# Optimization experiments

Hardware: AMD Instinct MI355X
Metric: run time of the kernel (lower is better)

## Reference

```python
import jax, jax.numpy as jnp
import numpy as np

B = 4096
ED = 128          # EMBEDDING_DIM
HD = 64           # HIDDEN_DIM
LH = 128          # LSTM_HIDDEN_DIM
IN_DIM = ED * (12 + 48 + 1)  # 7808
N_ABILITY, N_MOVE = 300, 900


def setup_inputs() -> dict:
    key = jax.random.key(0)
    ks = jax.random.split(key, 16)
    s = lambda k, shape, scale=0.05: (jax.random.normal(k, shape, dtype=jnp.float32) * scale)
    return {
        "ability_ids": jax.random.randint(ks[0], (B, 12), 0, N_ABILITY),
        "move_ids": jax.random.randint(ks[1], (B, 48), 0, N_MOVE),
        "numerical": s(ks[2], (B, 84), 1.0),
        "mask": (jax.random.uniform(ks[3], (B, 9)) > 0.3).astype(jnp.float32),
        "h0": jnp.zeros((B, LH), jnp.float32),
        "c0": jnp.zeros((B, LH), jnp.float32),
        "ability_emb": s(ks[4], (N_ABILITY, ED), 1.0),
        "move_emb": s(ks[5], (N_MOVE, ED), 1.0),
        "num_W": s(ks[6], (ED, 84)),
        "num_b": s(ks[7], (ED,)),
        "Wih": s(ks[8], (4 * LH, IN_DIM), 0.01),
        "Whh": s(ks[9], (4 * LH, LH)),
        "bih": s(ks[10], (4 * LH,)),
        "bhh": s(ks[11], (4 * LH,)),
        "W1": s(ks[12], (HD, LH)),
        "b1": s(ks[13], (HD,)),
        "W2": s(ks[14], (ED, HD)),
        "b2": s(ks[15], (ED,)),
        "Wa": s(jax.random.fold_in(key, 100), (9, ED)),
        "ba": s(jax.random.fold_in(key, 101), (9,)),
    }


def reference(ability_ids, move_ids, numerical, mask, h0, c0,
              ability_emb, move_emb, num_W, num_b,
              Wih, Whh, bih, bhh, W1, b1, W2, b2, Wa, ba):
    # Gather + concat: [B, 12*ED] + [B, 48*ED] + [B, ED] -> [B, 7808]
    ab = ability_emb[ability_ids].reshape(ability_ids.shape[0], 12 * ED)
    mv = move_emb[move_ids].reshape(move_ids.shape[0], 48 * ED)
    num = numerical @ num_W.T + num_b
    x = jnp.concatenate([ab, mv, num], axis=-1)

    # Single-timestep LSTM (torch gate order: i, f, g, o)
    gates = x @ Wih.T + bih + h0 @ Whh.T + bhh
    i, f, g, o = jnp.split(gates, 4, axis=-1)
    i, f, o = jax.nn.sigmoid(i), jax.nn.sigmoid(f), jax.nn.sigmoid(o)
    g = jnp.tanh(g)
    c1 = f * c0 + i * g
    h1 = o * jnp.tanh(c1)

    # MLP head + action logits
    feat = jax.nn.relu(h1 @ W1.T + b1) @ W2.T + b2
    probs = jax.nn.softmax(feat @ Wa.T + ba, axis=-1)

    # Masked renormalization; fall back to unmasked probs when mask kills everything
    masked = probs * mask
    ssum = masked.sum(-1, keepdims=True)
    out = jnp.where(ssum > 0, masked / jnp.where(ssum > 0, ssum, 1.0), probs)
    return out, h1, c1
```

## Files before the change

### kernel.cpp

```cpp
#include <hip/hip_runtime.h>
#include <hip/hip_bf16.h>
#include <stdint.h>
#include <stddef.h>

typedef __bf16 bf16;
typedef __bf16 bf16x8 __attribute__((ext_vector_type(8)));
typedef float f32x4 __attribute__((ext_vector_type(4)));

#define BATCH 4096
#define KIH 7808
#define KTOT 7936
#define NG 512
#define LH 128
#define HD 64
#define ED 128
#define SPLITK 4

#define OFF_WCAT 0u
#define OFF_GPART 8126464u
#define OFF_XT   41680896u
#define OFF_AB   43778048u
#define OFF_MV   43854848u
#define OFF_ADDR 44085248u
#define OFF_H1B  46182400u

#define O_H1 (BATCH * 9)
#define O_C1 (BATCH * 9 + BATCH * LH)

typedef const __attribute__((address_space(1))) uint32_t* gas_ptr;
typedef __attribute__((address_space(3))) uint32_t* las_ptr;

__device__ __forceinline__ void async16(const void* g, void* l) {
    __builtin_amdgcn_global_load_lds((gas_ptr)g, (las_ptr)l, 16, 0, 0);
}

__global__ void convert_w(const float* __restrict__ Wih,
                          const float* __restrict__ Whh,
                          bf16* __restrict__ Wcat) {
    const int n = blockIdx.x;
    const int t = threadIdx.x;
    const float* src_ih = Wih + (size_t)n * KIH;
    const float* src_hh = Whh + (size_t)n * LH;
    bf16* dst = Wcat + (size_t)n * KTOT;
    for (int k4 = t; k4 < KTOT / 4; k4 += 256) {
        const int k = k4 * 4;
        const float4 v = (k < KIH) ? *(const float4*)(src_ih + k)
                                   : *(const float4*)(src_hh + (k - KIH));
        bf16 o0 = (bf16)v.x, o1 = (bf16)v.y, o2 = (bf16)v.z, o3 = (bf16)v.w;
        dst[k] = o0; dst[k + 1] = o1; dst[k + 2] = o2; dst[k + 3] = o3;
    }
}

__global__ void convert_emb(const float* __restrict__ ab_emb,
                            const float* __restrict__ mv_emb,
                            bf16* __restrict__ ab8,
                            bf16* __restrict__ mv8) {
    const int i = blockIdx.x * 256 + threadIdx.x;
    if (i < 300 * 128) ab8[i] = (bf16)ab_emb[i];
    else mv8[i - 300 * 128] = (bf16)mv_emb[i - 300 * 128];
}

__global__ void build_pre(const int* __restrict__ ab_ids,
                          const int* __restrict__ mv_ids,
                          const float* __restrict__ numerical,
                          const float* __restrict__ h0,
                          const float* __restrict__ numW,
                          const float* __restrict__ numb,
                          bf16* __restrict__ xtail,
                          uint32_t* __restrict__ addrs) {
    const int b = blockIdx.x;
    const int t = threadIdx.x;

    __shared__ int ids[60];
    __shared__ float numr[84];
    if (t < 60) ids[t] = (t < 12) ? ab_ids[b * 12 + t] : mv_ids[b * 48 + (t - 12)];
    if (t >= 128 && t < 128 + 84) numr[t - 128] = numerical[(size_t)b * 84 + (t - 128)];
    __syncthreads();

    if (t < 128) {
        float acc = numb[t];
#pragma unroll 4
        for (int k = 0; k < 84; ++k)
            acc += numr[k] * numW[t * 84 + k];
        xtail[(size_t)b * 256 + t] = (bf16)acc;
    } else {
        const int tt = t - 128;
        xtail[(size_t)b * 256 + 128 + tt] = (bf16)h0[(size_t)b * LH + tt];
    }

    if (t < 64) {
        uint32_t off;
        if (t < 12) off = OFF_AB + (uint32_t)ids[t] * 256u;
        else if (t < 60) off = OFF_MV + (uint32_t)ids[t] * 256u;
        else if (t == 60) off = OFF_XT + (uint32_t)b * 512u;
        else if (t == 61) off = OFF_XT + (uint32_t)b * 512u + 256u;
        else off = OFF_XT;
        addrs[(size_t)b * 64 + t] = off;
    }
}

__global__ __launch_bounds__(256, 2) void gemm_gates(
    const uint8_t* __restrict__ wsbase,
    const bf16* __restrict__ Wcat,
    const uint32_t* __restrict__ addrs,
    float* __restrict__ gpart) {
    __shared__ bf16 As[2][128 * 64];
    __shared__ bf16 Bs[2][128 * 64];
    __shared__ uint32_t adr[17][128];

    const int tid = threadIdx.x;
    const int w = tid >> 6;
    const int lane = tid & 63;
    const int bm = blockIdx.x;
    const int bn = blockIdx.y;
    const int bz = blockIdx.z;
    const int kt_beg = bz * 31;
    const int kt_end = kt_beg + 31;

    const int s0 = kt_beg >> 1;
    const int ns = ((kt_end - 1) >> 1) - s0 + 1;
    for (int i = tid; i < ns * 128; i += 256) {
        adr[i >> 7][i & 127] =
            addrs[(size_t)(bm * 128 + (i & 127)) * 64 + s0 + (i >> 7)];
    }

    const int r_l = lane >> 3;
    const int sc16 = ((lane & 7) ^ r_l) * 16;

    f32x4 acc[4][4];
#pragma unroll
    for (int i = 0; i < 4; ++i)
#pragma unroll
        for (int j = 0; j < 4; ++j)
#pragma unroll
            for (int r = 0; r < 4; ++r) acc[i][j][r] = 0.f;

    const int m0 = (w & 1) * 64;
    const int n0 = (w >> 1) * 64;

    __syncthreads();

    auto stage = [&](int kt, int pb) {
        const int k0 = kt * 64;
        const int sl = (kt >> 1) - s0;
        const int hb = (kt & 1) * 128;
#pragma unroll
        for (int j = 0; j < 4; ++j) {
            const int row = (w * 4 + j) * 8 + r_l;
            const uint8_t* gsrc = wsbase + adr[sl][row] + hb + sc16;
            async16(gsrc, (void*)&As[pb][((w * 4 + j) * 64 + lane) * 8]);
        }
#pragma unroll
        for (int j = 0; j < 4; ++j) {
            const int row = (w * 4 + j) * 8 + r_l;
            const bf16* gsrc = Wcat + (size_t)(bn * 128 + row) * KTOT + k0 + (sc16 >> 1);
            async16(gsrc, (void*)&Bs[pb][((w * 4 + j) * 64 + lane) * 8]);
        }
    };

    stage(kt_beg, 0);

    for (int kt = kt_beg; kt < kt_end; ++kt) {
        const int pb = (kt - kt_beg) & 1;
        __syncthreads();
        if (kt + 1 < kt_end) stage(kt + 1, pb ^ 1);

        const bf16* Ab = &As[pb][0];
        const bf16* Bb = &Bs[pb][0];
#pragma unroll
        for (int ks = 0; ks < 2; ++ks) {
            bf16x8 af[4], bfr[4];
            const int kk8 = ks * 4 + (lane >> 4);
#pragma unroll
            for (int t = 0; t < 4; ++t) {
                const int m = m0 + t * 16 + (lane & 15);
                af[t] = *(const bf16x8*)&Ab[m * 64 + ((kk8 ^ (m & 7)) * 8)];
                const int n = n0 + t * 16 + (lane & 15);
                bfr[t] = *(const bf16x8*)&Bb[n * 64 + ((kk8 ^ (n & 7)) * 8)];
            }
#pragma unroll
            for (int ti = 0; ti < 4; ++ti)
#pragma unroll
                for (int tj = 0; tj < 4; ++tj)
                    acc[ti][tj] = __builtin_amdgcn_mfma_f32_16x16x32_bf16(
                        af[ti], bfr[tj], acc[ti][tj], 0, 0, 0);
        }
    }

    float* gdst = gpart + (size_t)bz * BATCH * NG;
    const int mlo = (lane >> 4) * 4;
    const int nlo = lane & 15;
#pragma unroll
    for (int ti = 0; ti < 4; ++ti)
#pragma unroll
        for (int tj = 0; tj < 4; ++tj) {
            const int mg = bm * 128 + m0 + ti * 16 + mlo;
            const int ng = bn * 128 + n0 + tj * 16 + nlo;
            float* dst = gdst + (size_t)mg * NG + ng;
#pragma unroll
            for (int r = 0; r < 4; ++r)
                dst[(size_t)r * NG] = acc[ti][tj][r];
        }
}

__global__ void reduce_lstm(const float* __restrict__ gpart,
                            const float* __restrict__ bih,
                            const float* __restrict__ bhh,
                            const float* __restrict__ c0,
                            float* __restrict__ out,
                            bf16* __restrict__ h1b) {
    const int t = threadIdx.x;
    const int b = blockIdx.x * 2 + (t >> 7);
    const int u = t & 127;

    float gv[4];
#pragma unroll
    for (int q = 0; q < 4; ++q)
        gv[q] = bih[q * 128 + u] + bhh[q * 128 + u];
#pragma unroll
    for (int z = 0; z < SPLITK; ++z) {
        const float* gz = gpart + ((size_t)z * BATCH + b) * NG + u;
#pragma unroll
        for (int q = 0; q < 4; ++q) gv[q] += gz[q * 128];
    }

    const float iv = 1.f / (1.f + __expf(-gv[0]));
    const float fv = 1.f / (1.f + __expf(-gv[1]));
    const float gg = tanhf(gv[2]);
    const float ov = 1.f / (1.f + __expf(-gv[3]));
    const float c1 = fv * c0[(size_t)b * LH + u] + iv * gg;
    const float h1 = ov * tanhf(c1);

    out[O_H1 + (size_t)b * LH + u] = h1;
    out[O_C1 + (size_t)b * LH + u] = c1;
    h1b[(size_t)b * LH + u] = (bf16)h1;
}

__global__ __launch_bounds__(128, 2) void mlp_head(
    const bf16* __restrict__ h1b, const float* __restrict__ mask,
    const float* __restrict__ W1, const float* __restrict__ b1,
    const float* __restrict__ W2, const float* __restrict__ b2,
    const float* __restrict__ Wa, const float* __restrict__ ba,
    float* __restrict__ out) {
    __shared__ bf16 W1f[8192];
    __shared__ bf16 W2f[8192];
    __shared__ bf16 Waf[2048];
    __shared__ bf16 uS[2][16 * 64];
    __shared__ bf16 fS[2][16 * 128];
    __shared__ float b1s[64];
    __shared__ float b2s[128];
    __shared__ float bas[16];

    const int tid = threadIdx.x;
    for (int e = tid; e < 8192; e += 128) {
        const int j = e & 7, ln = (e >> 3) & 63, fid = e >> 9;
        const int kt = fid & 3, nt = fid >> 2;
        const int n = nt * 16 + (ln & 15);
        const int k = kt * 32 + (ln >> 4) * 8 + j;
        W1f[e] = (bf16)W1[n * 128 + k];
    }
    for (int e = tid; e < 8192; e += 128) {
        const int j = e & 7, ln = (e >> 3) & 63, fid = e >> 9;
        const int kt = fid & 1, nt = fid >> 1;
        const int n = nt * 16 + (ln & 15);
        const int k = kt * 32 + (ln >> 4) * 8 + j;
        W2f[e] = (bf16)W2[n * 64 + k];
    }
    for (int e = tid; e < 2048; e += 128) {
        const int j = e & 7, ln = (e >> 3) & 63, kt = e >> 9;
        const int n = ln & 15;
        const int k = kt * 32 + (ln >> 4) * 8 + j;
        Waf[e] = (n < 9) ? (bf16)Wa[n * 128 + k] : (bf16)0.f;
    }
    if (tid < 64) b1s[tid] = b1[tid];
    if (tid < 16) bas[tid] = (tid < 9) ? ba[tid] : 0.f;
    {
        const int i = tid;
        if (i < 128) b2s[i] = b2[i];
    }
    __syncthreads();

    const int wv = tid >> 6, lane = tid & 63;
    const int mt = blockIdx.x * 2 + wv;
    const int mrow0 = mt * 16;
    const int nl = lane & 15, kg = lane >> 4;

    bf16x8 ah[4];
#pragma unroll
    for (int kt = 0; kt < 4; ++kt)
        ah[kt] = *(const bf16x8*)&h1b[(size_t)(mrow0 + nl) * 128 + kt * 32 + kg * 8];

#pragma unroll
    for (int nt = 0; nt < 4; ++nt) {
        f32x4 a = {0.f, 0.f, 0.f, 0.f};
#pragma unroll
        for (int kt = 0; kt < 4; ++kt)
            a = __builtin_amdgcn_mfma_f32_16x16x32_bf16(
                ah[kt], *(const bf16x8*)&W1f[((nt * 4 + kt) * 64 + lane) * 8], a, 0, 0, 0);
        const int n = nt * 16 + nl;
#pragma unroll
        for (int r = 0; r < 4; ++r)
            uS[wv][(kg * 4 + r) * 64 + n] = (bf16)fmaxf(a[r] + b1s[n], 0.f);
    }

    bf16x8 au[2];
#pragma unroll
    for (int kt = 0; kt < 2; ++kt)
        au[kt] = *(const bf16x8*)&uS[wv][nl * 64 + kt * 32 + kg * 8];

#pragma unroll
    for (int nt = 0; nt < 8; ++nt) {
        f32x4 a = {0.f, 0.f, 0.f, 0.f};
#pragma unroll
        for (int kt = 0; kt < 2; ++kt)
            a = __builtin_amdgcn_mfma_f32_16x16x32_bf16(
                au[kt], *(const bf16x8*)&W2f[((nt * 2 + kt) * 64 + lane) * 8], a, 0, 0, 0);
        const int n = nt * 16 + nl;
#pragma unroll
        for (int r = 0; r < 4; ++r)
            fS[wv][(kg * 4 + r) * 128 + n] = (bf16)(a[r] + b2s[n]);
    }

    bf16x8 afr[4];
#pragma unroll
    for (int kt = 0; kt < 4; ++kt)
        afr[kt] = *(const bf16x8*)&fS[wv][nl * 128 + kt * 32 + kg * 8];

    f32x4 lg4 = {0.f, 0.f, 0.f, 0.f};
#pragma unroll
    for (int kt = 0; kt < 4; ++kt)
        lg4 = __builtin_amdgcn_mfma_f32_16x16x32_bf16(
            afr[kt], *(const bf16x8*)&Waf[(kt * 64 + lane) * 8], lg4, 0, 0, 0);

#pragma unroll
    for (int r = 0; r < 4; ++r) {
        const int b = mrow0 + kg * 4 + r;
        float lg = (nl < 9) ? lg4[r] + bas[nl] : -1e30f;
        float mx = lg;
#pragma unroll
        for (int off = 1; off < 16; off <<= 1)
            mx = fmaxf(mx, __shfl_xor(mx, off, 64));
        const float e = (nl < 9) ? __expf(lg - mx) : 0.f;
        const float mv = (nl < 9) ? mask[(size_t)b * 9 + nl] : 0.f;
        float tot = e, ms = e * mv;
#pragma unroll
        for (int off = 1; off < 16; off <<= 1) {
            tot += __shfl_xor(tot, off, 64);
            ms += __shfl_xor(ms, off, 64);
        }
        if (nl < 9)
            out[(size_t)b * 9 + nl] = (ms > 0.f) ? e * mv / ms : e / tot;
    }
}

extern "C" void kernel_launch(void* const* d_in, const int* in_sizes, int n_in,
                              void* d_out, int out_size, void* d_ws, size_t ws_size,
                              hipStream_t stream) {
    const int* ab_ids = (const int*)d_in[0];
    const int* mv_ids = (const int*)d_in[1];
    const float* numerical = (const float*)d_in[2];
    const float* mask = (const float*)d_in[3];
    const float* h0 = (const float*)d_in[4];
    const float* c0 = (const float*)d_in[5];
    const float* ab_emb = (const float*)d_in[6];
    const float* mv_emb = (const float*)d_in[7];
    const float* numW = (const float*)d_in[8];
    const float* numb = (const float*)d_in[9];
    const float* Wih = (const float*)d_in[10];
    const float* Whh = (const float*)d_in[11];
    const float* bih = (const float*)d_in[12];
    const float* bhh = (const float*)d_in[13];
    const float* W1 = (const float*)d_in[14];
    const float* b1 = (const float*)d_in[15];
    const float* W2 = (const float*)d_in[16];
    const float* b2 = (const float*)d_in[17];
    const float* Wa = (const float*)d_in[18];
    const float* ba = (const float*)d_in[19];
    float* out = (float*)d_out;

    uint8_t* ws = (uint8_t*)d_ws;
    bf16* Wcat = (bf16*)(ws + OFF_WCAT);
    float* gpart = (float*)(ws + OFF_GPART);
    bf16* xtail = (bf16*)(ws + OFF_XT);
    bf16* ab8 = (bf16*)(ws + OFF_AB);
    bf16* mv8 = (bf16*)(ws + OFF_MV);
    uint32_t* addrs = (uint32_t*)(ws + OFF_ADDR);
    bf16* h1b = (bf16*)(ws + OFF_H1B);

    convert_w<<<512, 256, 0, stream>>>(Wih, Whh, Wcat);
    convert_emb<<<600, 256, 0, stream>>>(ab_emb, mv_emb, ab8, mv8);
    build_pre<<<BATCH, 256, 0, stream>>>(ab_ids, mv_ids, numerical, h0,
                                         numW, numb, xtail, addrs);
    gemm_gates<<<dim3(32, 4, SPLITK), 256, 0, stream>>>(ws, Wcat, addrs, gpart);
    reduce_lstm<<<BATCH / 2, 256, 0, stream>>>(gpart, bih, bhh, c0, out, h1b);
    mlp_head<<<128, 128, 0, stream>>>(h1b, mask, W1, b1, W2, b2, Wa, ba, out);
}
```

Before: 190.7 us.

## Merge prep kernels, enlarge GEMM M-tile, fuse LSTM reduce into MLP head

Merges the three preprocessing kernels (weight convert, embedding convert, build_pre) into one launch that dispatches on block index. The gates GEMM moves to 512-thread blocks with a 256-row M tile, so each B tile is reused across twice as many rows. The split-K reduction and LSTM cell are fused into the MLP head kernel, which keeps h1 in shared memory instead of writing it to workspace. This removes launch overhead and a global round trip. The cost is more shared memory and registers per GEMM block, and a tail kernel of only 256 blocks that redoes the weight staging in each block.

```diff
diff --git a/kernel.cpp b/kernel.cpp
--- a/kernel.cpp
+++ b/kernel.cpp
@@ -22,7 +22,6 @@
 #define OFF_AB   43778048u
 #define OFF_MV   43854848u
 #define OFF_ADDR 44085248u
-#define OFF_H1B  46182400u
 
 #define O_H1 (BATCH * 9)
 #define O_C1 (BATCH * 9 + BATCH * LH)
@@ -34,79 +33,81 @@
     __builtin_amdgcn_global_load_lds((gas_ptr)g, (las_ptr)l, 16, 0, 0);
 }
 
-__global__ void convert_w(const float* __restrict__ Wih,
-                          const float* __restrict__ Whh,
-                          bf16* __restrict__ Wcat) {
-    const int n = blockIdx.x;
+__global__ void prep(const int* __restrict__ ab_ids,
+                     const int* __restrict__ mv_ids,
+                     const float* __restrict__ numerical,
+                     const float* __restrict__ h0,
+                     const float* __restrict__ numW,
+                     const float* __restrict__ numb,
+                     const float* __restrict__ Wih,
+                     const float* __restrict__ Whh,
+                     const float* __restrict__ ab_emb,
+                     const float* __restrict__ mv_emb,
+                     uint8_t* __restrict__ ws) {
+    const int bid = blockIdx.x;
     const int t = threadIdx.x;
-    const float* src_ih = Wih + (size_t)n * KIH;
-    const float* src_hh = Whh + (size_t)n * LH;
-    bf16* dst = Wcat + (size_t)n * KTOT;
-    for (int k4 = t; k4 < KTOT / 4; k4 += 256) {
-        const int k = k4 * 4;
-        const float4 v = (k < KIH) ? *(const float4*)(src_ih + k)
-                                   : *(const float4*)(src_hh + (k - KIH));
-        bf16 o0 = (bf16)v.x, o1 = (bf16)v.y, o2 = (bf16)v.z, o3 = (bf16)v.w;
-        dst[k] = o0; dst[k + 1] = o1; dst[k + 2] = o2; dst[k + 3] = o3;
-    }
-}
-
-__global__ void convert_emb(const float* __restrict__ ab_emb,
-                            const float* __restrict__ mv_emb,
-                            bf16* __restrict__ ab8,
-                            bf16* __restrict__ mv8) {
-    const int i = blockIdx.x * 256 + threadIdx.x;
-    if (i < 300 * 128) ab8[i] = (bf16)ab_emb[i];
-    else mv8[i - 300 * 128] = (bf16)mv_emb[i - 300 * 128];
-}
-
-__global__ void build_pre(const int* __restrict__ ab_ids,
-                          const int* __restrict__ mv_ids,
-                          const float* __restrict__ numerical,
-                          const float* __restrict__ h0,
-                          const float* __restrict__ numW,
-                          const float* __restrict__ numb,
-                          bf16* __restrict__ xtail,
-                          uint32_t* __restrict__ addrs) {
-    const int b = blockIdx.x;
-    const int t = threadIdx.x;
-
-    __shared__ int ids[60];
-    __shared__ float numr[84];
-    if (t < 60) ids[t] = (t < 12) ? ab_ids[b * 12 + t] : mv_ids[b * 48 + (t - 12)];
-    if (t >= 128 && t < 128 + 84) numr[t - 128] = numerical[(size_t)b * 84 + (t - 128)];
-    __syncthreads();
-
-    if (t < 128) {
-        float acc = numb[t];
+
+    if (bid < BATCH) {
+        bf16* xtail = (bf16*)(ws + OFF_XT);
+        uint32_t* addrs = (uint32_t*)(ws + OFF_ADDR);
+        const int b = bid;
+
+        __shared__ int ids[60];
+        __shared__ float numr[84];
+        if (t < 60) ids[t] = (t < 12) ? ab_ids[b * 12 + t] : mv_ids[b * 48 + (t - 12)];
+        if (t >= 128 && t < 128 + 84) numr[t - 128] = numerical[(size_t)b * 84 + (t - 128)];
+        __syncthreads();
+
+        if (t < 128) {
+            float acc = numb[t];
 #pragma unroll 4
-        for (int k = 0; k < 84; ++k)
-            acc += numr[k] * numW[t * 84 + k];
-        xtail[(size_t)b * 256 + t] = (bf16)acc;
+            for (int k = 0; k < 84; ++k)
+                acc += numr[k] * numW[t * 84 + k];
+            xtail[(size_t)b * 256 + t] = (bf16)acc;
+        } else {
+            const int tt = t - 128;
+            xtail[(size_t)b * 256 + 128 + tt] = (bf16)h0[(size_t)b * LH + tt];
+        }
+
+        if (t < 64) {
+            uint32_t off;
+            if (t < 12) off = OFF_AB + (uint32_t)ids[t] * 256u;
+            else if (t < 60) off = OFF_MV + (uint32_t)ids[t] * 256u;
+            else if (t == 60) off = OFF_XT + (uint32_t)b * 512u;
+            else if (t == 61) off = OFF_XT + (uint32_t)b * 512u + 256u;
+            else off = OFF_XT;
+            addrs[(size_t)b * 64 + t] = off;
+        }
+    } else if (bid < BATCH + 512) {
+        bf16* Wcat = (bf16*)(ws + OFF_WCAT);
+        const int n = bid - BATCH;
+        const float* src_ih = Wih + (size_t)n * KIH;
+        const float* src_hh = Whh + (size_t)n * LH;
+        bf16* dst = Wcat + (size_t)n * KTOT;
+        for (int k4 = t; k4 < KTOT / 4; k4 += 256) {
+            const int k = k4 * 4;
+            const float4 v = (k < KIH) ? *(const float4*)(src_ih + k)
+                                       : *(const float4*)(src_hh + (k - KIH));
+            bf16 o0 = (bf16)v.x, o1 = (bf16)v.y, o2 = (bf16)v.z, o3 = (bf16)v.w;
+            dst[k] = o0; dst[k + 1] = o1; dst[k + 2] = o2; dst[k + 3] = o3;
+        }
     } else {
-        const int tt = t - 128;
-        xtail[(size_t)b * 256 + 128 + tt] = (bf16)h0[(size_t)b * LH + tt];
-    }
-
-    if (t < 64) {
-        uint32_t off;
-        if (t < 12) off = OFF_AB + (uint32_t)ids[t] * 256u;
-        else if (t < 60) off = OFF_MV + (uint32_t)ids[t] * 256u;
-        else if (t == 60) off = OFF_XT + (uint32_t)b * 512u;
-        else if (t == 61) off = OFF_XT + (uint32_t)b * 512u + 256u;
-        else off = OFF_XT;
-        addrs[(size_t)b * 64 + t] = off;
-    }
-}
-
-__global__ __launch_bounds__(256, 2) void gemm_gates(
+        bf16* ab8 = (bf16*)(ws + OFF_AB);
+        bf16* mv8 = (bf16*)(ws + OFF_MV);
+        const int i = (bid - BATCH - 512) * 256 + t;
+        if (i < 300 * 128) ab8[i] = (bf16)ab_emb[i];
+        else if (i < 1200 * 128) mv8[i - 300 * 128] = (bf16)mv_emb[i - 300 * 128];
+    }
+}
+
+__global__ __launch_bounds__(512, 2) void gemm_gates(
     const uint8_t* __restrict__ wsbase,
     const bf16* __restrict__ Wcat,
     const uint32_t* __restrict__ addrs,
     float* __restrict__ gpart) {
-    __shared__ bf16 As[2][128 * 64];
+    __shared__ bf16 As[2][256 * 64];
     __shared__ bf16 Bs[2][128 * 64];
-    __shared__ uint32_t adr[17][128];
+    __shared__ uint32_t adr[16][256];
 
     const int tid = threadIdx.x;
     const int w = tid >> 6;
@@ -119,9 +120,9 @@
 
     const int s0 = kt_beg >> 1;
     const int ns = ((kt_end - 1) >> 1) - s0 + 1;
-    for (int i = tid; i < ns * 128; i += 256) {
-        adr[i >> 7][i & 127] =
-            addrs[(size_t)(bm * 128 + (i & 127)) * 64 + s0 + (i >> 7)];
+    for (int i = tid; i < ns * 256; i += 512) {
+        adr[i >> 8][i & 255] =
+            addrs[(size_t)(bm * 256 + (i & 255)) * 64 + s0 + (i >> 8)];
     }
 
     const int r_l = lane >> 3;
@@ -135,8 +136,9 @@
 #pragma unroll
             for (int r = 0; r < 4; ++r) acc[i][j][r] = 0.f;
 
-    const int m0 = (w & 1) * 64;
-    const int n0 = (w >> 1) * 64;
+    const int wm = w & 3, wn = w >> 2;
+    const int m0 = wm * 64;
+    const int n0 = wn * 64;
 
     __syncthreads();
 
@@ -146,15 +148,17 @@
         const int hb = (kt & 1) * 128;
 #pragma unroll
         for (int j = 0; j < 4; ++j) {
-            const int row = (w * 4 + j) * 8 + r_l;
+            const int g = w * 4 + j;
+            const int row = g * 8 + r_l;
             const uint8_t* gsrc = wsbase + adr[sl][row] + hb + sc16;
-            async16(gsrc, (void*)&As[pb][((w * 4 + j) * 64 + lane) * 8]);
-        }
-#pragma unroll
-        for (int j = 0; j < 4; ++j) {
-            const int row = (w * 4 + j) * 8 + r_l;
+            async16(gsrc, (void*)&As[pb][(g * 64 + lane) * 8]);
+        }
+#pragma unroll
+        for (int j = 0; j < 2; ++j) {
+            const int g = w * 2 + j;
+            const int row = g * 8 + r_l;
             const bf16* gsrc = Wcat + (size_t)(bn * 128 + row) * KTOT + k0 + (sc16 >> 1);
-            async16(gsrc, (void*)&Bs[pb][((w * 4 + j) * 64 + lane) * 8]);
+            async16(gsrc, (void*)&Bs[pb][(g * 64 + lane) * 8]);
         }
     };
 
@@ -194,7 +198,7 @@
     for (int ti = 0; ti < 4; ++ti)
 #pragma unroll
         for (int tj = 0; tj < 4; ++tj) {
-            const int mg = bm * 128 + m0 + ti * 16 + mlo;
+            const int mg = bm * 256 + m0 + ti * 16 + mlo;
             const int ng = bn * 128 + n0 + tj * 16 + nlo;
             float* dst = gdst + (size_t)mg * NG + ng;
 #pragma unroll
@@ -203,41 +207,10 @@
         }
 }
 
-__global__ void reduce_lstm(const float* __restrict__ gpart,
-                            const float* __restrict__ bih,
-                            const float* __restrict__ bhh,
-                            const float* __restrict__ c0,
-                            float* __restrict__ out,
-                            bf16* __restrict__ h1b) {
-    const int t = threadIdx.x;
-    const int b = blockIdx.x * 2 + (t >> 7);
-    const int u = t & 127;
-
-    float gv[4];
-#pragma unroll
-    for (int q = 0; q < 4; ++q)
-        gv[q] = bih[q * 128 + u] + bhh[q * 128 + u];
-#pragma unroll
-    for (int z = 0; z < SPLITK; ++z) {
-        const float* gz = gpart + ((size_t)z * BATCH + b) * NG + u;
-#pragma unroll
-        for (int q = 0; q < 4; ++q) gv[q] += gz[q * 128];
-    }
-
-    const float iv = 1.f / (1.f + __expf(-gv[0]));
-    const float fv = 1.f / (1.f + __expf(-gv[1]));
-    const float gg = tanhf(gv[2]);
-    const float ov = 1.f / (1.f + __expf(-gv[3]));
-    const float c1 = fv * c0[(size_t)b * LH + u] + iv * gg;
-    const float h1 = ov * tanhf(c1);
-
-    out[O_H1 + (size_t)b * LH + u] = h1;
-    out[O_C1 + (size_t)b * LH + u] = c1;
-    h1b[(size_t)b * LH + u] = (bf16)h1;
-}
-
-__global__ __launch_bounds__(128, 2) void mlp_head(
-    const bf16* __restrict__ h1b, const float* __restrict__ mask,
+__global__ __launch_bounds__(128, 3) void tail(
+    const float* __restrict__ gpart, const float* __restrict__ bih,
+    const float* __restrict__ bhh, const float* __restrict__ c0,
+    const float* __restrict__ mask,
     const float* __restrict__ W1, const float* __restrict__ b1,
     const float* __restrict__ W2, const float* __restrict__ b2,
     const float* __restrict__ Wa, const float* __restrict__ ba,
@@ -245,13 +218,16 @@
     __shared__ bf16 W1f[8192];
     __shared__ bf16 W2f[8192];
     __shared__ bf16 Waf[2048];
-    __shared__ bf16 uS[2][16 * 64];
-    __shared__ bf16 fS[2][16 * 128];
+    __shared__ bf16 h1s[16 * 128];
+    __shared__ bf16 uS[16 * 64];
+    __shared__ bf16 fS[16 * 128];
     __shared__ float b1s[64];
     __shared__ float b2s[128];
     __shared__ float bas[16];
 
     const int tid = threadIdx.x;
+    const int b0 = blockIdx.x * 16;
+
     for (int e = tid; e < 8192; e += 128) {
         const int j = e & 7, ln = (e >> 3) & 63, fid = e >> 9;
         const int kt = fid & 3, nt = fid >> 2;
@@ -274,24 +250,47 @@
     }
     if (tid < 64) b1s[tid] = b1[tid];
     if (tid < 16) bas[tid] = (tid < 9) ? ba[tid] : 0.f;
-    {
-        const int i = tid;
-        if (i < 128) b2s[i] = b2[i];
+    if (tid < 128) b2s[tid] = b2[tid];
+
+#pragma unroll
+    for (int i = 0; i < 16; ++i) {
+        const int p = tid + 128 * i;
+        const int uu = p & 127;
+        const int r = p >> 7;
+        const int b = b0 + r;
+        float gv[4];
+#pragma unroll
+        for (int q = 0; q < 4; ++q)
+            gv[q] = bih[q * 128 + uu] + bhh[q * 128 + uu];
+#pragma unroll
+        for (int z = 0; z < SPLITK; ++z) {
+            const float* gz = gpart + ((size_t)z * BATCH + b) * NG + uu;
+#pragma unroll
+            for (int q = 0; q < 4; ++q) gv[q] += gz[q * 128];
+        }
+        const float iv = 1.f / (1.f + __expf(-gv[0]));
+        const float fv = 1.f / (1.f + __expf(-gv[1]));
+        const float gg = tanhf(gv[2]);
+        const float ov = 1.f / (1.f + __expf(-gv[3]));
+        const float c1 = fv * c0[(size_t)b * LH + uu] + iv * gg;
+        const float h1 = ov * tanhf(c1);
+        out[O_H1 + (size_t)b * LH + uu] = h1;
+        out[O_C1 + (size_t)b * LH + uu] = c1;
+        h1s[r * 128 + uu] = (bf16)h1;
     }
     __syncthreads();
 
     const int wv = tid >> 6, lane = tid & 63;
-    const int mt = blockIdx.x * 2 + wv;
-    const int mrow0 = mt * 16;
     const int nl = lane & 15, kg = lane >> 4;
 
     bf16x8 ah[4];
 #pragma unroll
     for (int kt = 0; kt < 4; ++kt)
-        ah[kt] = *(const bf16x8*)&h1b[(size_t)(mrow0 + nl) * 128 + kt * 32 + kg * 8];
-
-#pragma unroll
-    for (int nt = 0; nt < 4; ++nt) {
+        ah[kt] = *(const bf16x8*)&h1s[nl * 128 + kt * 32 + kg * 8];
+
+#pragma unroll
+    for (int t2 = 0; t2 < 2; ++t2) {
+        const int nt = wv * 2 + t2;
         f32x4 a = {0.f, 0.f, 0.f, 0.f};
 #pragma unroll
         for (int kt = 0; kt < 4; ++kt)
@@ -300,16 +299,18 @@
         const int n = nt * 16 + nl;
 #pragma unroll
         for (int r = 0; r < 4; ++r)
-            uS[wv][(kg * 4 + r) * 64 + n] = (bf16)fmaxf(a[r] + b1s[n], 0.f);
-    }
+            uS[(kg * 4 + r) * 64 + n] = (bf16)fmaxf(a[r] + b1s[n], 0.f);
+    }
+    __syncthreads();
 
     bf16x8 au[2];
 #pragma unroll
     for (int kt = 0; kt < 2; ++kt)
-        au[kt] = *(const bf16x8*)&uS[wv][nl * 64 + kt * 32 + kg * 8];
-
-#pragma unroll
-    for (int nt = 0; nt < 8; ++nt) {
+        au[kt] = *(const bf16x8*)&uS[nl * 64 + kt * 32 + kg * 8];
+
+#pragma unroll
+    for (int t2 = 0; t2 < 4; ++t2) {
+        const int nt = wv * 4 + t2;
         f32x4 a = {0.f, 0.f, 0.f, 0.f};
 #pragma unroll
         for (int kt = 0; kt < 2; ++kt)
@@ -318,38 +319,41 @@
         const int n = nt * 16 + nl;
 #pragma unroll
         for (int r = 0; r < 4; ++r)
-            fS[wv][(kg * 4 + r) * 128 + n] = (bf16)(a[r] + b2s[n]);
-    }
-
-    bf16x8 afr[4];
-#pragma unroll
-    for (int kt = 0; kt < 4; ++kt)
-        afr[kt] = *(const bf16x8*)&fS[wv][nl * 128 + kt * 32 + kg * 8];
-
-    f32x4 lg4 = {0.f, 0.f, 0.f, 0.f};
-#pragma unroll
-    for (int kt = 0; kt < 4; ++kt)
-        lg4 = __builtin_amdgcn_mfma_f32_16x16x32_bf16(
-            afr[kt], *(const bf16x8*)&Waf[(kt * 64 + lane) * 8], lg4, 0, 0, 0);
-
-#pragma unroll
-    for (int r = 0; r < 4; ++r) {
-        const int b = mrow0 + kg * 4 + r;
-        float lg = (nl < 9) ? lg4[r] + bas[nl] : -1e30f;
-        float mx = lg;
-#pragma unroll
-        for (int off = 1; off < 16; off <<= 1)
-            mx = fmaxf(mx, __shfl_xor(mx, off, 64));
-        const float e = (nl < 9) ? __expf(lg - mx) : 0.f;
-        const float mv = (nl < 9) ? mask[(size_t)b * 9 + nl] : 0.f;
-        float tot = e, ms = e * mv;
-#pragma unroll
-        for (int off = 1; off < 16; off <<= 1) {
-            tot += __shfl_xor(tot, off, 64);
-            ms += __shfl_xor(ms, off, 64);
-        }
-        if (nl < 9)
-            out[(size_t)b * 9 + nl] = (ms > 0.f) ? e * mv / ms : e / tot;
+            fS[(kg * 4 + r) * 128 + n] = (bf16)(a[r] + b2s[n]);
+    }
+    __syncthreads();
+
+    if (wv == 0) {
+        bf16x8 afr[4];
+#pragma unroll
+        for (int kt = 0; kt < 4; ++kt)
+            afr[kt] = *(const bf16x8*)&fS[nl * 128 + kt * 32 + kg * 8];
+
+        f32x4 lg4 = {0.f, 0.f, 0.f, 0.f};
+#pragma unroll
+        for (int kt = 0; kt < 4; ++kt)
+            lg4 = __builtin_amdgcn_mfma_f32_16x16x32_bf16(
+                afr[kt], *(const bf16x8*)&Waf[(kt * 64 + lane) * 8], lg4, 0, 0, 0);
+
+#pragma unroll
+        for (int r = 0; r < 4; ++r) {
+            const int b = b0 + kg * 4 + r;
+            float lg = (nl < 9) ? lg4[r] + bas[nl] : -1e30f;
+            float mx = lg;
+#pragma unroll
+            for (int off = 1; off < 16; off <<= 1)
+                mx = fmaxf(mx, __shfl_xor(mx, off, 64));
+            const float e = (nl < 9) ? __expf(lg - mx) : 0.f;
+            const float mv = (nl < 9) ? mask[(size_t)b * 9 + nl] : 0.f;
+            float tot = e, ms = e * mv;
+#pragma unroll
+            for (int off = 1; off < 16; off <<= 1) {
+                tot += __shfl_xor(tot, off, 64);
+                ms += __shfl_xor(ms, off, 64);
+            }
+            if (nl < 9)
+                out[(size_t)b * 9 + nl] = (ms > 0.f) ? e * mv / ms : e / tot;
+        }
     }
 }
 
@@ -381,17 +385,11 @@
     uint8_t* ws = (uint8_t*)d_ws;
     bf16* Wcat = (bf16*)(ws + OFF_WCAT);
     float* gpart = (float*)(ws + OFF_GPART);
-    bf16* xtail = (bf16*)(ws + OFF_XT);
-    bf16* ab8 = (bf16*)(ws + OFF_AB);
-    bf16* mv8 = (bf16*)(ws + OFF_MV);
     uint32_t* addrs = (uint32_t*)(ws + OFF_ADDR);
-    bf16* h1b = (bf16*)(ws + OFF_H1B);
-
-    convert_w<<<512, 256, 0, stream>>>(Wih, Whh, Wcat);
-    convert_emb<<<600, 256, 0, stream>>>(ab_emb, mv_emb, ab8, mv8);
-    build_pre<<<BATCH, 256, 0, stream>>>(ab_ids, mv_ids, numerical, h0,
-                                         numW, numb, xtail, addrs);
-    gemm_gates<<<dim3(32, 4, SPLITK), 256, 0, stream>>>(ws, Wcat, addrs, gpart);
-    reduce_lstm<<<BATCH / 2, 256, 0, stream>>>(gpart, bih, bhh, c0, out, h1b);
-    mlp_head<<<128, 128, 0, stream>>>(h1b, mask, W1, b1, W2, b2, Wa, ba, out);
-}
+
+    prep<<<BATCH + 512 + 600, 256, 0, stream>>>(
+        ab_ids, mv_ids, numerical, h0, numW, numb, Wih, Whh, ab_emb, mv_emb, ws);
+    gemm_gates<<<dim3(16, 4, SPLITK), 512, 0, stream>>>(ws, Wcat, addrs, gpart);
+    tail<<<BATCH / 16, 128, 0, stream>>>(gpart, bih, bhh, c0, mask,
+                                         W1, b1, W2, b2, Wa, ba, out);
+}
```

Result: slower. 195.3 us (+2.4%).

## Fuse preprocessing kernels and pre-swizzle MLP head weights once in workspace

Applied to the files above, without the earlier changes.

Merges the weight conversion, embedding conversion and per-row pre-build kernels into a single prep launch, dispatched by block index ranges. A dedicated block in that launch also converts and swizzles the W1/W2/Wa MLP weights into the workspace, so mlp_head no longer rebuilds them in LDS in every block. mlp_head becomes 256 single-wave blocks that read fragments straight from global memory, with bias loads from global. This removes two launches and redundant per-block weight staging, at the cost of a serial single-block weight prep and uncached global fragment reads.

```diff
diff --git a/kernel.cpp b/kernel.cpp
--- a/kernel.cpp
+++ b/kernel.cpp
@@ -23,6 +23,9 @@
 #define OFF_MV   43854848u
 #define OFF_ADDR 44085248u
 #define OFF_H1B  46182400u
+#define OFF_W1F  47230976u
+#define OFF_W2F  47247360u
+#define OFF_WAF  47263744u
 
 #define O_H1 (BATCH * 9)
 #define O_C1 (BATCH * 9 + BATCH * LH)
@@ -34,68 +37,97 @@
     __builtin_amdgcn_global_load_lds((gas_ptr)g, (las_ptr)l, 16, 0, 0);
 }
 
-__global__ void convert_w(const float* __restrict__ Wih,
-                          const float* __restrict__ Whh,
-                          bf16* __restrict__ Wcat) {
-    const int n = blockIdx.x;
+__global__ void prep(const int* __restrict__ ab_ids,
+                     const int* __restrict__ mv_ids,
+                     const float* __restrict__ numerical,
+                     const float* __restrict__ h0,
+                     const float* __restrict__ numW,
+                     const float* __restrict__ numb,
+                     const float* __restrict__ Wih,
+                     const float* __restrict__ Whh,
+                     const float* __restrict__ ab_emb,
+                     const float* __restrict__ mv_emb,
+                     const float* __restrict__ W1,
+                     const float* __restrict__ W2,
+                     const float* __restrict__ Wa,
+                     uint8_t* __restrict__ ws) {
+    const int bid = blockIdx.x;
     const int t = threadIdx.x;
-    const float* src_ih = Wih + (size_t)n * KIH;
-    const float* src_hh = Whh + (size_t)n * LH;
-    bf16* dst = Wcat + (size_t)n * KTOT;
-    for (int k4 = t; k4 < KTOT / 4; k4 += 256) {
-        const int k = k4 * 4;
-        const float4 v = (k < KIH) ? *(const float4*)(src_ih + k)
-                                   : *(const float4*)(src_hh + (k - KIH));
-        bf16 o0 = (bf16)v.x, o1 = (bf16)v.y, o2 = (bf16)v.z, o3 = (bf16)v.w;
-        dst[k] = o0; dst[k + 1] = o1; dst[k + 2] = o2; dst[k + 3] = o3;
-    }
-}
-
-__global__ void convert_emb(const float* __restrict__ ab_emb,
-                            const float* __restrict__ mv_emb,
-                            bf16* __restrict__ ab8,
-                            bf16* __restrict__ mv8) {
-    const int i = blockIdx.x * 256 + threadIdx.x;
-    if (i < 300 * 128) ab8[i] = (bf16)ab_emb[i];
-    else mv8[i - 300 * 128] = (bf16)mv_emb[i - 300 * 128];
-}
-
-__global__ void build_pre(const int* __restrict__ ab_ids,
-                          const int* __restrict__ mv_ids,
-                          const float* __restrict__ numerical,
-                          const float* __restrict__ h0,
-                          const float* __restrict__ numW,
-                          const float* __restrict__ numb,
-                          bf16* __restrict__ xtail,
-                          uint32_t* __restrict__ addrs) {
-    const int b = blockIdx.x;
-    const int t = threadIdx.x;
-
-    __shared__ int ids[60];
-    __shared__ float numr[84];
-    if (t < 60) ids[t] = (t < 12) ? ab_ids[b * 12 + t] : mv_ids[b * 48 + (t - 12)];
-    if (t >= 128 && t < 128 + 84) numr[t - 128] = numerical[(size_t)b * 84 + (t - 128)];
-    __syncthreads();
-
-    if (t < 128) {
-        float acc = numb[t];
+
+    if (bid < BATCH) {
+        bf16* xtail = (bf16*)(ws + OFF_XT);
+        uint32_t* addrs = (uint32_t*)(ws + OFF_ADDR);
+        const int b = bid;
+
+        __shared__ int ids[60];
+        __shared__ float numr[84];
+        if (t < 60) ids[t] = (t < 12) ? ab_ids[b * 12 + t] : mv_ids[b * 48 + (t - 12)];
+        if (t >= 128 && t < 128 + 84) numr[t - 128] = numerical[(size_t)b * 84 + (t - 128)];
+        __syncthreads();
+
+        if (t < 128) {
+            float acc = numb[t];
 #pragma unroll 4
-        for (int k = 0; k < 84; ++k)
-            acc += numr[k] * numW[t * 84 + k];
-        xtail[(size_t)b * 256 + t] = (bf16)acc;
+            for (int k = 0; k < 84; ++k)
+                acc += numr[k] * numW[t * 84 + k];
+            xtail[(size_t)b * 256 + t] = (bf16)acc;
+        } else {
+            const int tt = t - 128;
+            xtail[(size_t)b * 256 + 128 + tt] = (bf16)h0[(size_t)b * LH + tt];
+        }
+
+        if (t < 64) {
+            uint32_t off;
+            if (t < 12) off = OFF_AB + (uint32_t)ids[t] * 256u;
+            else if (t < 60) off = OFF_MV + (uint32_t)ids[t] * 256u;
+            else if (t == 60) off = OFF_XT + (uint32_t)b * 512u;
+            else if (t == 61) off = OFF_XT + (uint32_t)b * 512u + 256u;
+            else off = OFF_XT;
+            addrs[(size_t)b * 64 + t] = off;
+        }
+    } else if (bid < BATCH + 512) {
+        bf16* Wcat = (bf16*)(ws + OFF_WCAT);
+        const int n = bid - BATCH;
+        const float* src_ih = Wih + (size_t)n * KIH;
+        const float* src_hh = Whh + (size_t)n * LH;
+        bf16* dst = Wcat + (size_t)n * KTOT;
+        for (int k4 = t; k4 < KTOT / 4; k4 += 256) {
+            const int k = k4 * 4;
+            const float4 v = (k < KIH) ? *(const float4*)(src_ih + k)
+                                       : *(const float4*)(src_hh + (k - KIH));
+            bf16 o0 = (bf16)v.x, o1 = (bf16)v.y, o2 = (bf16)v.z, o3 = (bf16)v.w;
+            dst[k] = o0; dst[k + 1] = o1; dst[k + 2] = o2; dst[k + 3] = o3;
+        }
+    } else if (bid < BATCH + 512 + 600) {
+        bf16* ab8 = (bf16*)(ws + OFF_AB);
+        bf16* mv8 = (bf16*)(ws + OFF_MV);
+        const int i = (bid - BATCH - 512) * 256 + t;
+        if (i < 300 * 128) ab8[i] = (bf16)ab_emb[i];
+        else if (i < 1200 * 128) mv8[i - 300 * 128] = (bf16)mv_emb[i - 300 * 128];
     } else {
-        const int tt = t - 128;
-        xtail[(size_t)b * 256 + 128 + tt] = (bf16)h0[(size_t)b * LH + tt];
-    }
-
-    if (t < 64) {
-        uint32_t off;
-        if (t < 12) off = OFF_AB + (uint32_t)ids[t] * 256u;
-        else if (t < 60) off = OFF_MV + (uint32_t)ids[t] * 256u;
-        else if (t == 60) off = OFF_XT + (uint32_t)b * 512u;
-        else if (t == 61) off = OFF_XT + (uint32_t)b * 512u + 256u;
-        else off = OFF_XT;
-        addrs[(size_t)b * 64 + t] = off;
+        bf16* W1f = (bf16*)(ws + OFF_W1F);
+        bf16* W2f = (bf16*)(ws + OFF_W2F);
+        bf16* Waf = (bf16*)(ws + OFF_WAF);
+        for (int e = t; e < 8192; e += 256) {
+            const int j = e & 7, ln = (e >> 3) & 63, fid = e >> 9;
+            const int kt = fid & 3, nt = fid >> 2;
+            const int n = nt * 16 + (ln & 15);
+            const int k = kt * 32 + (ln >> 4) * 8 + j;
+            W1f[e] = (bf16)W1[n * 128 + k];
+        }
+        for (int e = t; e < 8192; e += 256) {
+            const int j = e & 7, ln = (e >> 3) & 63, fid = e >> 9;
+            const int kt = fid & 1, nt = fid >> 1;
+            const int n = nt * 16 + (ln & 15);
+            const int k = kt * 32 + (ln >> 4) * 8 + j;
+            W2f[e] = (bf16)W2[n * 64 + k];
+        }
+        for (int e = t; e < 2048; e += 256) {
+            const int j = e & 7, ln = (e >> 3) & 63, kt = e >> 9;
+            const int n = ln & 15;
+            const int k = kt * 32 + (ln >> 4) * 8 + j;
+            Waf[e] = (n < 9) ? (bf16)Wa[n * 128 + k] : (bf16)0.f;
+        }
     }
 }
 
@@ -236,59 +268,24 @@
     h1b[(size_t)b * LH + u] = (bf16)h1;
 }
 
-__global__ __launch_bounds__(128, 2) void mlp_head(
+__global__ __launch_bounds__(64) void mlp_head(
     const bf16* __restrict__ h1b, const float* __restrict__ mask,
-    const float* __restrict__ W1, const float* __restrict__ b1,
-    const float* __restrict__ W2, const float* __restrict__ b2,
-    const float* __restrict__ Wa, const float* __restrict__ ba,
+    const bf16* __restrict__ W1f, const bf16* __restrict__ W2f,
+    const bf16* __restrict__ Waf,
+    const float* __restrict__ b1, const float* __restrict__ b2,
+    const float* __restrict__ ba,
     float* __restrict__ out) {
-    __shared__ bf16 W1f[8192];
-    __shared__ bf16 W2f[8192];
-    __shared__ bf16 Waf[2048];
-    __shared__ bf16 uS[2][16 * 64];
-    __shared__ bf16 fS[2][16 * 128];
-    __shared__ float b1s[64];
-    __shared__ float b2s[128];
-    __shared__ float bas[16];
-
-    const int tid = threadIdx.x;
-    for (int e = tid; e < 8192; e += 128) {
-        const int j = e & 7, ln = (e >> 3) & 63, fid = e >> 9;
-        const int kt = fid & 3, nt = fid >> 2;
-        const int n = nt * 16 + (ln & 15);
-        const int k = kt * 32 + (ln >> 4) * 8 + j;
-        W1f[e] = (bf16)W1[n * 128 + k];
-    }
-    for (int e = tid; e < 8192; e += 128) {
-        const int j = e & 7, ln = (e >> 3) & 63, fid = e >> 9;
-        const int kt = fid & 1, nt = fid >> 1;
-        const int n = nt * 16 + (ln & 15);
-        const int k = kt * 32 + (ln >> 4) * 8 + j;
-        W2f[e] = (bf16)W2[n * 64 + k];
-    }
-    for (int e = tid; e < 2048; e += 128) {
-        const int j = e & 7, ln = (e >> 3) & 63, kt = e >> 9;
-        const int n = ln & 15;
-        const int k = kt * 32 + (ln >> 4) * 8 + j;
-        Waf[e] = (n < 9) ? (bf16)Wa[n * 128 + k] : (bf16)0.f;
-    }
-    if (tid < 64) b1s[tid] = b1[tid];
-    if (tid < 16) bas[tid] = (tid < 9) ? ba[tid] : 0.f;
-    {
-        const int i = tid;
-        if (i < 128) b2s[i] = b2[i];
-    }
-    __syncthreads();
-
-    const int wv = tid >> 6, lane = tid & 63;
-    const int mt = blockIdx.x * 2 + wv;
-    const int mrow0 = mt * 16;
+    __shared__ bf16 uS[16 * 64];
+    __shared__ bf16 fS[16 * 128];
+
+    const int lane = threadIdx.x;
+    const int b0 = blockIdx.x * 16;
     const int nl = lane & 15, kg = lane >> 4;
 
     bf16x8 ah[4];
 #pragma unroll
     for (int kt = 0; kt < 4; ++kt)
-        ah[kt] = *(const bf16x8*)&h1b[(size_t)(mrow0 + nl) * 128 + kt * 32 + kg * 8];
+        ah[kt] = *(const bf16x8*)&h1b[(size_t)(b0 + nl) * 128 + kt * 32 + kg * 8];
 
 #pragma unroll
     for (int nt = 0; nt < 4; ++nt) {
@@ -296,17 +293,20 @@
 #pragma unroll
         for (int kt = 0; kt < 4; ++kt)
             a = __builtin_amdgcn_mfma_f32_16x16x32_bf16(
-                ah[kt], *(const bf16x8*)&W1f[((nt * 4 + kt) * 64 + lane) * 8], a, 0, 0, 0);
+                ah[kt], *(const bf16x8*)&W1f[((nt * 4 + kt) * 64 + lane) * 8],
+                a, 0, 0, 0);
         const int n = nt * 16 + nl;
+        const float bb = b1[n];
 #pragma unroll
         for (int r = 0; r < 4; ++r)
-            uS[wv][(kg * 4 + r) * 64 + n] = (bf16)fmaxf(a[r] + b1s[n], 0.f);
-    }
+            uS[(kg * 4 + r) * 64 + n] = (bf16)fmaxf(a[r] + bb, 0.f);
+    }
+    __syncthreads();
 
     bf16x8 au[2];
 #pragma unroll
     for (int kt = 0; kt < 2; ++kt)
-        au[kt] = *(const bf16x8*)&uS[wv][nl * 64 + kt * 32 + kg * 8];
+        au[kt] = *(const bf16x8*)&uS[nl * 64 + kt * 32 + kg * 8];
 
 #pragma unroll
     for (int nt = 0; nt < 8; ++nt) {
@@ -314,17 +314,20 @@
 #pragma unroll
         for (int kt = 0; kt < 2; ++kt)
             a = __builtin_amdgcn_mfma_f32_16x16x32_bf16(
-                au[kt], *(const bf16x8*)&W2f[((nt * 2 + kt) * 64 + lane) * 8], a, 0, 0, 0);
+                au[kt], *(const bf16x8*)&W2f[((nt * 2 + kt) * 64 + lane) * 8],
+                a, 0, 0, 0);
         const int n = nt * 16 + nl;
+        const float bb = b2[n];
 #pragma unroll
         for (int r = 0; r < 4; ++r)
-            fS[wv][(kg * 4 + r) * 128 + n] = (bf16)(a[r] + b2s[n]);
-    }
+            fS[(kg * 4 + r) * 128 + n] = (bf16)(a[r] + bb);
+    }
+    __syncthreads();
 
     bf16x8 afr[4];
 #pragma unroll
     for (int kt = 0; kt < 4; ++kt)
-        afr[kt] = *(const bf16x8*)&fS[wv][nl * 128 + kt * 32 + kg * 8];
+        afr[kt] = *(const bf16x8*)&fS[nl * 128 + kt * 32 + kg * 8];
 
     f32x4 lg4 = {0.f, 0.f, 0.f, 0.f};
 #pragma unroll
@@ -332,10 +335,12 @@
         lg4 = __builtin_amdgcn_mfma_f32_16x16x32_bf16(
             afr[kt], *(const bf16x8*)&Waf[(kt * 64 + lane) * 8], lg4, 0, 0, 0);
 
+    const float bav = (nl < 9) ? ba[nl] : 0.f;
+
 #pragma unroll
     for (int r = 0; r < 4; ++r) {
-        const int b = mrow0 + kg * 4 + r;
-        float lg = (nl < 9) ? lg4[r] + bas[nl] : -1e30f;
+        const int b = b0 + kg * 4 + r;
+        float lg = (nl < 9) ? lg4[r] + bav : -1e30f;
         float mx = lg;
 #pragma unroll
         for (int off = 1; off < 16; off <<= 1)
@@ -381,17 +386,17 @@
     uint8_t* ws = (uint8_t*)d_ws;
     bf16* Wcat = (bf16*)(ws + OFF_WCAT);
     float* gpart = (float*)(ws + OFF_GPART);
-    bf16* xtail = (bf16*)(ws + OFF_XT);
-    bf16* ab8 = (bf16*)(ws + OFF_AB);
-    bf16* mv8 = (bf16*)(ws + OFF_MV);
     uint32_t* addrs = (uint32_t*)(ws + OFF_ADDR);
     bf16* h1b = (bf16*)(ws + OFF_H1B);
-
-    convert_w<<<512, 256, 0, stream>>>(Wih, Whh, Wcat);
-    convert_emb<<<600, 256, 0, stream>>>(ab_emb, mv_emb, ab8, mv8);
-    build_pre<<<BATCH, 256, 0, stream>>>(ab_ids, mv_ids, numerical, h0,
-                                         numW, numb, xtail, addrs);
+    bf16* W1f = (bf16*)(ws + OFF_W1F);
+    bf16* W2f = (bf16*)(ws + OFF_W2F);
+    bf16* Waf = (bf16*)(ws + OFF_WAF);
+
+    prep<<<BATCH + 512 + 600 + 1, 256, 0, stream>>>(
+        ab_ids, mv_ids, numerical, h0, numW, numb, Wih, Whh, ab_emb, mv_emb,
+        W1, W2, Wa, ws);
     gemm_gates<<<dim3(32, 4, SPLITK), 256, 0, stream>>>(ws, Wcat, addrs, gpart);
     reduce_lstm<<<BATCH / 2, 256, 0, stream>>>(gpart, bih, bhh, c0, out, h1b);
-    mlp_head<<<128, 128, 0, stream>>>(h1b, mask, W1, b1, W2, b2, Wa, ba, out);
-}
+    mlp_head<<<BATCH / 16, 64, 0, stream>>>(h1b, mask, W1f, W2f, Waf,
+                                            b1, b2, ba, out);
+}
```

After: 182.2 us. 4.4% less time.
